# Kernel optimization log

Measured on AMD Instinct MI355X. Metric: run time of the kernel, lower is better.

The kernel has to match this reference:

```python
import jax, jax.numpy as jnp
import numpy as np

DIM = 128
N_GNN = 3
B, N1, N2 = 8, 128, 512
VDW_N = 6.0
DEV_VDW = 0.2
MAX_VDW, MIN_VDW = 0.0356, 0.0178
DM_MIN = 0.5


def setup_inputs() -> dict:
    key = jax.random.key(0)
    ks = jax.random.split(key, 24)
    f32 = jnp.float32
    h1 = jax.random.normal(ks[0], (B, N1, 54), f32)
    h2 = jax.random.normal(ks[1], (B, N2, 54), f32)
    a1 = (jax.random.uniform(ks[2], (B, N1, N1)) < 0.1).astype(f32)
    adj1 = jnp.clip(a1 + jnp.swapaxes(a1, 1, 2) + jnp.eye(N1, dtype=f32), 0.0, 1.0)
    a2 = (jax.random.uniform(ks[3], (B, N2, N2)) < 0.05).astype(f32)
    adj2 = jnp.clip(a2 + jnp.swapaxes(a2, 1, 2) + jnp.eye(N2, dtype=f32), 0.0, 1.0)
    A_int = (jax.random.uniform(ks[4], (B, 8, N1, N2)) < 0.05).astype(f32)
    pos1 = jax.random.uniform(ks[5], (B, N1, 3), f32) * 30.0
    pos2 = jax.random.uniform(ks[6], (B, N2, 3), f32) * 30.0
    rotor = jax.random.uniform(ks[7], (B,), f32) * 10.0
    vdw_radius1 = 1.0 + jax.random.uniform(ks[8], (B, N1), f32)
    vdw_radius2 = 1.0 + jax.random.uniform(ks[9], (B, N2), f32)
    delta_uff = jax.random.uniform(ks[10], (B,), f32)
    no_metal1 = jnp.ones((B, N1), f32)
    no_metal2 = jnp.ones((B, N2), f32)
    s = 0.1
    node_W = jax.random.normal(ks[11], (54, DIM), f32) * s
    gat_W = jax.random.normal(ks[12], (N_GNN, DIM, DIM), f32) * s
    gat_b = jnp.zeros((N_GNN, DIM), f32)
    gat_A = jax.random.normal(ks[13], (N_GNN, DIM, DIM), f32) * s
    gate_W = jax.random.normal(ks[14], (N_GNN, 2 * DIM), f32) * s
    gate_b = jnp.zeros((N_GNN,), f32)
    vdwA_W1 = jax.random.normal(ks[15], (2 * DIM, 128), f32) * s
    vdwA_b1 = jnp.zeros((128,), f32)
    vdwA_W2 = jax.random.normal(ks[16], (128,), f32) * s
    vdwA_b2 = jnp.zeros((1,), f32)
    vdwB_W1 = jax.random.normal(ks[17], (2 * DIM, 128), f32) * s
    vdwB_b1 = jnp.zeros((128,), f32)
    vdwB_W2 = jax.random.normal(ks[18], (128,), f32) * s
    vdwB_b2 = jnp.zeros((1,), f32)
    hbond_coeff = jnp.array([1.0], f32)
    hydrophobic_coeff = jnp.array([0.5], f32)
    vdw_coeff = jnp.array([1.0], f32)
    rotor_coeff = jnp.array([0.5], f32)
    return dict(h1=h1, adj1=adj1, h2=h2, adj2=adj2, A_int=A_int, pos1=pos1, pos2=pos2,
                rotor=rotor, vdw_radius1=vdw_radius1, vdw_radius2=vdw_radius2,
                delta_uff=delta_uff, no_metal1=no_metal1, no_metal2=no_metal2,
                node_W=node_W, gat_W=gat_W, gat_b=gat_b, gat_A=gat_A, gate_W=gate_W,
                gate_b=gate_b, vdwA_W1=vdwA_W1, vdwA_b1=vdwA_b1, vdwA_W2=vdwA_W2,
                vdwA_b2=vdwA_b2, vdwB_W1=vdwB_W1, vdwB_b1=vdwB_b1, vdwB_W2=vdwB_W2,
                vdwB_b2=vdwB_b2, hbond_coeff=hbond_coeff,
                hydrophobic_coeff=hydrophobic_coeff, vdw_coeff=vdw_coeff,
                rotor_coeff=rotor_coeff)


def _gat(x, adj, W, b, A, gW, gb):
    # PIGNet GAT_gate: attention softmax over axis=1, masked by adj, gated residual.
    h = x @ W + b                                   # [B,N,D]
    e = jnp.einsum('bil,bkl->bik', h @ A, h)        # [B,N,N]
    e = e + jnp.swapaxes(e, 1, 2)
    att = jnp.where(adj > 0, e, -9e15)
    att = jax.nn.softmax(att, axis=1) * adj
    h_prime = jax.nn.relu(jnp.einsum('bij,bjk->bik', att, h))
    coeff = jax.nn.sigmoid(jnp.concatenate([x, h_prime], -1) @ gW + gb)[..., None]
    return coeff * x + (1.0 - coeff) * h_prime


def _pair_mlp(g1, g2, W1, b1, w2, b2):
    # Equivalent to Linear(cat[h1_rep,h2_rep]) without materializing the 2D concat.
    z = (jnp.einsum('bik,kh->bih', g1, W1[:DIM])[:, :, None, :]
         + jnp.einsum('bjk,kh->bjh', g2, W1[DIM:])[:, None, :, :] + b1)  # [B,N1,N2,128]
    return jax.nn.relu(z) @ w2 + b2                 # [B,N1,N2]


def _forward(h1, adj1, h2, adj2, A_int, pos1, pos2, rotor, vdw_radius1, vdw_radius2,
             delta_uff, no_metal1, no_metal2, node_W, gat_W, gat_b, gat_A, gate_W,
             gate_b, vdwA_W1, vdwA_b1, vdwA_W2, vdwA_b2, vdwB_W1, vdwB_b1, vdwB_W2,
             vdwB_b2, hbond_coeff, hydrophobic_coeff, vdw_coeff, rotor_coeff):
    g1 = h1 @ node_W
    g2 = h2 @ node_W
    for i in range(N_GNN):
        g1 = _gat(g1, adj1, gat_W[i], gat_b[i], gat_A[i], gate_W[i], gate_b[i])
        g2 = _gat(g2, adj2, gat_W[i], gat_b[i], gat_A[i], gate_W[i], gate_b[i])
    diff = pos1[:, :, None, :] - pos2[:, None, :, :]
    dm = jnp.sqrt(jnp.sum(diff * diff, -1) + 1e-10)   # [B,N1,N2]
    dm = jnp.where(dm < DM_MIN, 1e10, dm)
    A_w = jax.nn.sigmoid(_pair_mlp(g1, g2, vdwA_W1, vdwA_b1, vdwA_W2, vdwA_b2))
    B_w = jnp.tanh(_pair_mlp(g1, g2, vdwB_W1, vdwB_b1, vdwB_W2, vdwB_b2)) * DEV_VDW
    dm0 = vdw_radius1[:, :, None] + vdw_radius2[:, None, :] + B_w
    # vdW 12-6 term
    dm0_safe = jnp.where(dm0 < 1e-4, 1.0, dm0)
    rN = (dm0_safe / dm) ** VDW_N
    evdw = jnp.minimum(rN * rN - 2.0 * rN, 100.0)
    mask12 = no_metal1[:, :, None] * no_metal2[:, None, :]
    Aamp = A_w * (MAX_VDW - MIN_VDW) + MIN_VDW
    E_vdw = jnp.sum(Aamp * evdw * mask12, axis=(1, 2))
    # hbond / hydrophobic terms use unfixed dm0
    dmd = dm - dm0
    hb = -(hbond_coeff * hbond_coeff)[0]
    hy = -(hydrophobic_coeff * hydrophobic_coeff)[0]
    E_hb1 = jnp.sum(jnp.clip(dmd * A_int[:, 1] / -0.7, 0.0, 1.0), axis=(1, 2)) * hb
    E_hb2 = jnp.sum(jnp.clip(dmd * A_int[:, -1] / -0.7, 0.0, 1.0), axis=(1, 2)) * hb
    E_hp = jnp.sum(jnp.clip((-dmd + 1.5) * A_int[:, -2], 0.0, 1.0), axis=(1, 2)) * hy
    E_t = delta_uff * (vdw_coeff * vdw_coeff)[0]
    ret = jnp.stack([E_vdw, E_hb1, E_hb2, E_hp, E_t], -1)   # [B,5]
    ret = ret / (1.0 + (rotor_coeff * rotor_coeff)[0] * rotor[:, None])
    return ret


def reference(h1, adj1, h2, adj2, A_int, pos1, pos2, rotor, vdw_radius1, vdw_radius2,
              delta_uff, no_metal1, no_metal2, node_W, gat_W, gat_b, gat_A, gate_W,
              gate_b, vdwA_W1, vdwA_b1, vdwA_W2, vdwA_b2, vdwB_W1, vdwB_b1, vdwB_W2,
              vdwB_b2, hbond_coeff, hydrophobic_coeff, vdw_coeff, rotor_coeff):
    return _forward(h1, adj1, h2, adj2, A_int, pos1, pos2, rotor, vdw_radius1,
                    vdw_radius2, delta_uff, no_metal1, no_metal2, node_W, gat_W,
                    gat_b, gat_A, gate_W, gate_b, vdwA_W1, vdwA_b1, vdwA_W2,
                    vdwA_b2, vdwB_W1, vdwB_b1, vdwB_W2, vdwB_b2, hbond_coeff,
                    hydrophobic_coeff, vdw_coeff, rotor_coeff)
```

## Files before the change

kernel.cpp:

```cpp
#include <hip/hip_runtime.h>
#include <math.h>

#define D 128
#define NB 8
#define NN1 128
#define NN2 512
#define ROWS1 (NB * NN1)
#define ROWS2 (NB * NN2)
#define ROWS (ROWS1 + ROWS2)
#define CAP1 96
#define CAP2 160
#define CSR_ELEMS ((size_t)ROWS1 * CAP1 + (size_t)ROWS2 * CAP2)

__device__ __forceinline__ void resolve_row(int row, int& base_row, size_t& cbase,
                                            int& N) {
    if (row < ROWS1) {
        base_row = row & ~127;
        cbase = (size_t)row * CAP1;
        N = NN1;
    } else {
        int r = row - ROWS1;
        base_row = ROWS1 + (r & ~511);
        cbase = (size_t)ROWS1 * CAP1 + (size_t)r * CAP2;
        N = NN2;
    }
}

__global__ __launch_bounds__(128) void k_csrembed(
    const float* __restrict__ h1, const float* __restrict__ h2,
    const float* __restrict__ adj1, const float* __restrict__ adj2,
    const float* __restrict__ W, float* __restrict__ g,
    unsigned short* __restrict__ csr, int* __restrict__ nnz) {
    int row = blockIdx.x;
    int t = threadIdx.x;
    const float* src = (row < ROWS1) ? h1 + (size_t)row * 54
                                     : h2 + (size_t)(row - ROWS1) * 54;
    __shared__ float xr[56];
    if (t < 54) xr[t] = src[t];
    __syncthreads();
    float a0 = 0.f, a1 = 0.f;
#pragma unroll
    for (int k = 0; k < 54; k += 2) {
        a0 += xr[k] * W[k * D + t];
        if (k + 1 < 54) a1 += xr[k + 1] * W[(k + 1) * D + t];
    }
    g[(size_t)row * D + t] = a0 + a1;

    if (t < 64) {
        int base_row, N;
        size_t cbase;
        resolve_row(row, base_row, cbase, N);
        int cap = (row < ROWS1) ? CAP1 : CAP2;
        const float* arow = (row < ROWS1)
                                ? adj1 + (size_t)row * NN1
                                : adj2 + (size_t)(row - ROWS1) * NN2;
        int cnt = 0;
        for (int c0 = 0; c0 < N; c0 += 64) {
            float v = arow[c0 + t];
            unsigned long long m = __ballot(v > 0.f);
            int rank = __popcll(m & ((1ull << t) - 1ull));
            if (v > 0.f && cnt + rank < cap)
                csr[cbase + cnt + rank] = (unsigned short)(c0 + t);
            cnt += __popcll(m);
        }
        if (t == 0) nnz[row] = cnt < cap ? cnt : cap;
    }
}

__global__ __launch_bounds__(256) void k_h(const float* __restrict__ g,
                                           const float* __restrict__ W,
                                           const float* __restrict__ bias,
                                           const float* __restrict__ A,
                                           float* __restrict__ h, float* __restrict__ hA) {
    int row0 = blockIdx.x * 16;
    int t = threadIdx.x;
    int d = t & 127, rh = t >> 7;
    __shared__ float xs[16][D];
    __shared__ float hs[16][D];
    {
        int r = t >> 4, c = (t & 15) * 8;
        *(float4*)&xs[r][c] = *(const float4*)&g[((size_t)row0 + r) * D + c];
        *(float4*)&xs[r][c + 4] = *(const float4*)&g[((size_t)row0 + r) * D + c + 4];
    }
    __syncthreads();
    float bv = bias[d];
    float acc[8];
#pragma unroll
    for (int u = 0; u < 8; ++u) acc[u] = bv;
    for (int k0 = 0; k0 < D; k0 += 4) {
        float w0 = W[(k0 + 0) * D + d];
        float w1 = W[(k0 + 1) * D + d];
        float w2 = W[(k0 + 2) * D + d];
        float w3 = W[(k0 + 3) * D + d];
#pragma unroll
        for (int u = 0; u < 8; ++u) {
            float4 xv = *(const float4*)&xs[rh * 8 + u][k0];
            acc[u] += xv.x * w0 + xv.y * w1 + xv.z * w2 + xv.w * w3;
        }
    }
#pragma unroll
    for (int u = 0; u < 8; ++u) {
        int r = rh * 8 + u;
        h[((size_t)row0 + r) * D + d] = acc[u];
        hs[r][d] = acc[u];
    }
    __syncthreads();
    float acc2[8];
#pragma unroll
    for (int u = 0; u < 8; ++u) acc2[u] = 0.f;
    for (int k0 = 0; k0 < D; k0 += 4) {
        float w0 = A[(k0 + 0) * D + d];
        float w1 = A[(k0 + 1) * D + d];
        float w2 = A[(k0 + 2) * D + d];
        float w3 = A[(k0 + 3) * D + d];
#pragma unroll
        for (int u = 0; u < 8; ++u) {
            float4 xv = *(const float4*)&hs[rh * 8 + u][k0];
            acc2[u] += xv.x * w0 + xv.y * w1 + xv.z * w2 + xv.w * w3;
        }
    }
#pragma unroll
    for (int u = 0; u < 8; ++u)
        hA[((size_t)row0 + rh * 8 + u) * D + d] = acc2[u];
}

__global__ __launch_bounds__(128) void k_Ssp(const float* __restrict__ h,
                                             const float* __restrict__ hA,
                                             const unsigned short* __restrict__ csr,
                                             const int* __restrict__ nnz,
                                             float* __restrict__ svals,
                                             float2* __restrict__ rowstat) {
    int row = blockIdx.x;
    int t = threadIdx.x;
    int base_row, N;
    size_t cbase;
    resolve_row(row, base_row, cbase, N);
    int n = nnz[row];
    int grp = t >> 4, u = t & 15;
    const float* hrow = h + (size_t)row * D + u * 8;
    const float* hArow = hA + (size_t)row * D + u * 8;
    float4 hi0 = *(const float4*)&hrow[0], hi1 = *(const float4*)&hrow[4];
    float4 ai0 = *(const float4*)&hArow[0], ai1 = *(const float4*)&hArow[4];
    __shared__ float sv[CAP2];
    for (int s0 = 0; s0 < n; s0 += 8) {
        int s = s0 + grp;
        float p = 0.f;
        if (s < n) {
            int jrow = base_row + csr[cbase + s];
            const float* hj = h + (size_t)jrow * D + u * 8;
            const float* aj = hA + (size_t)jrow * D + u * 8;
            float4 hj0 = *(const float4*)&hj[0], hj1 = *(const float4*)&hj[4];
            float4 aj0 = *(const float4*)&aj[0], aj1 = *(const float4*)&aj[4];
            p = hi0.x * aj0.x + hi0.y * aj0.y + hi0.z * aj0.z + hi0.w * aj0.w +
                hi1.x * aj1.x + hi1.y * aj1.y + hi1.z * aj1.z + hi1.w * aj1.w +
                ai0.x * hj0.x + ai0.y * hj0.y + ai0.z * hj0.z + ai0.w * hj0.w +
                ai1.x * hj1.x + ai1.y * hj1.y + ai1.z * hj1.z + ai1.w * hj1.w;
        }
#pragma unroll
        for (int o = 8; o > 0; o >>= 1) p += __shfl_xor(p, o);
        if (s < n && u == 0) sv[s] = p;
    }
    __syncthreads();
    if (t < 64) {
        float m = -3.4e38f;
        for (int s = t; s < n; s += 64) m = fmaxf(m, sv[s]);
#pragma unroll
        for (int o = 32; o > 0; o >>= 1) m = fmaxf(m, __shfl_xor(m, o));
        float sum = 0.f;
        for (int s = t; s < n; s += 64) sum += expf(sv[s] - m);
#pragma unroll
        for (int o = 32; o > 0; o >>= 1) sum += __shfl_xor(sum, o);
        if (t == 0) rowstat[row] = make_float2(m, 1.f / sum);
    }
    for (int s = t; s < n; s += 128) svals[cbase + s] = sv[s];
}

__global__ __launch_bounds__(128) void k_hpgate(const float* __restrict__ hbuf,
                                                float* __restrict__ g,
                                                const float* __restrict__ svals,
                                                const float2* __restrict__ rowstat,
                                                const unsigned short* __restrict__ csr,
                                                const int* __restrict__ nnz,
                                                const float* __restrict__ gW,
                                                const float* __restrict__ gb) {
    int row = blockIdx.x;
    int d = threadIdx.x;
    int base_row, N;
    size_t cbase;
    resolve_row(row, base_row, cbase, N);
    int n = nnz[row];
    __shared__ float avals[CAP2];
    __shared__ int aidx[CAP2];
    __shared__ float red[128];
    for (int s = d; s < n; s += 128) {
        int jrow = base_row + csr[cbase + s];
        float2 st = rowstat[jrow];
        avals[s] = expf(svals[cbase + s] - st.x) * st.y;
        aidx[s] = jrow;
    }
    __syncthreads();
    float a0 = 0.f, a1 = 0.f, a2 = 0.f, a3 = 0.f;
    int s = 0;
    for (; s + 4 <= n; s += 4) {
        a0 += avals[s + 0] * hbuf[(size_t)aidx[s + 0] * D + d];
        a1 += avals[s + 1] * hbuf[(size_t)aidx[s + 1] * D + d];
        a2 += avals[s + 2] * hbuf[(size_t)aidx[s + 2] * D + d];
        a3 += avals[s + 3] * hbuf[(size_t)aidx[s + 3] * D + d];
    }
    for (; s < n; ++s) a0 += avals[s] * hbuf[(size_t)aidx[s] * D + d];
    float hv = fmaxf(a0 + a1 + a2 + a3, 0.f);
    float xv = g[(size_t)row * D + d];
    red[d] = xv * gW[d] + hv * gW[D + d];
    __syncthreads();
    for (int o = 64; o > 0; o >>= 1) {
        if (d < o) red[d] += red[d + o];
        __syncthreads();
    }
    float c = 1.f / (1.f + expf(-(red[0] + gb[0])));
    g[(size_t)row * D + d] = c * xv + (1.f - c) * hv;
}

__global__ __launch_bounds__(256) void k_pairpre(const float* __restrict__ g,
                                                 const float* __restrict__ WA,
                                                 const float* __restrict__ WB,
                                                 const float* __restrict__ bA,
                                                 const float* __restrict__ bB,
                                                 float* __restrict__ aA,
                                                 float* __restrict__ aB) {
    int row0 = blockIdx.x * 16;
    int t = threadIdx.x;
    int d = t & 127, rh = t >> 7;
    int g2 = (row0 >= ROWS1);
    const float* WAp = g2 ? WA + D * D : WA;
    const float* WBp = g2 ? WB + D * D : WB;
    __shared__ float xs[16][D];
    {
        int r = t >> 4, c = (t & 15) * 8;
        *(float4*)&xs[r][c] = *(const float4*)&g[((size_t)row0 + r) * D + c];
        *(float4*)&xs[r][c + 4] = *(const float4*)&g[((size_t)row0 + r) * D + c + 4];
    }
    __syncthreads();
    float bvA = g2 ? 0.f : bA[d];
    float bvB = g2 ? 0.f : bB[d];
    float accA[8], accB[8];
#pragma unroll
    for (int u = 0; u < 8; ++u) { accA[u] = bvA; accB[u] = bvB; }
    for (int k0 = 0; k0 < D; k0 += 4) {
        float wa0 = WAp[(k0 + 0) * D + d], wa1 = WAp[(k0 + 1) * D + d];
        float wa2 = WAp[(k0 + 2) * D + d], wa3 = WAp[(k0 + 3) * D + d];
        float wb0 = WBp[(k0 + 0) * D + d], wb1 = WBp[(k0 + 1) * D + d];
        float wb2 = WBp[(k0 + 2) * D + d], wb3 = WBp[(k0 + 3) * D + d];
#pragma unroll
        for (int u = 0; u < 8; ++u) {
            float4 xv = *(const float4*)&xs[rh * 8 + u][k0];
            accA[u] += xv.x * wa0 + xv.y * wa1 + xv.z * wa2 + xv.w * wa3;
            accB[u] += xv.x * wb0 + xv.y * wb1 + xv.z * wb2 + xv.w * wb3;
        }
    }
#pragma unroll
    for (int u = 0; u < 8; ++u) {
        int r = rh * 8 + u;
        aA[((size_t)row0 + r) * D + d] = accA[u];
        aB[((size_t)row0 + r) * D + d] = accB[u];
    }
}

__global__ __launch_bounds__(256) void k_pairz(
    const float* __restrict__ aA, const float* __restrict__ aB,
    const float* __restrict__ w2A, const float* __restrict__ w2B,
    const float* __restrict__ b2A, const float* __restrict__ b2B,
    const float* __restrict__ pos1, const float* __restrict__ pos2,
    const float* __restrict__ vr1, const float* __restrict__ vr2,
    const float* __restrict__ nm1, const float* __restrict__ nm2,
    const float* __restrict__ A_int, float* __restrict__ partials) {
    int b = blockIdx.y;
    int itile = blockIdx.x >> 4, jtile = blockIdx.x & 15;
    int i0 = itile * 32, j0 = jtile * 32;
    int t = threadIdx.x;
    int tx = t & 15, ty = t >> 4;
    __shared__ float A1a[32][20], A1b[32][20], A2a[32][20], A2b[32][20];
    __shared__ float w2As[128], w2Bs[128];
    __shared__ float zAs[32][33], zBs[32][33];
    if (t < 128) { w2As[t] = w2A[t]; w2Bs[t] = w2B[t]; }
    float zA[2][2] = {{0.f, 0.f}, {0.f, 0.f}};
    float zB[2][2] = {{0.f, 0.f}, {0.f, 0.f}};
    int half = t >> 7, idx = t & 127;
    int sr = idx >> 2, sc = (idx & 3) * 4;
    size_t grow = half ? (size_t)(ROWS1 + b * NN2 + j0 + sr)
                       : (size_t)(b * NN1 + i0 + sr);
    for (int hc = 0; hc < D; hc += 16) {
        __syncthreads();
        float4 va = *(const float4*)&aA[grow * D + hc + sc];
        float4 vb = *(const float4*)&aB[grow * D + hc + sc];
        if (half) { *(float4*)&A2a[sr][sc] = va; *(float4*)&A2b[sr][sc] = vb; }
        else      { *(float4*)&A1a[sr][sc] = va; *(float4*)&A1b[sr][sc] = vb; }
        __syncthreads();
#pragma unroll
        for (int hh = 0; hh < 16; hh += 4) {
            float4 wA = *(const float4*)&w2As[hc + hh];
            float4 wB = *(const float4*)&w2Bs[hc + hh];
            float4 xA0 = *(const float4*)&A1a[ty][hh];
            float4 xA1 = *(const float4*)&A1a[ty + 16][hh];
            float4 xB0 = *(const float4*)&A1b[ty][hh];
            float4 xB1 = *(const float4*)&A1b[ty + 16][hh];
            float4 yA0 = *(const float4*)&A2a[tx][hh];
            float4 yA1 = *(const float4*)&A2a[tx + 16][hh];
            float4 yB0 = *(const float4*)&A2b[tx][hh];
            float4 yB1 = *(const float4*)&A2b[tx + 16][hh];
#define RD4(xx, yy, ww) (fmaxf(xx.x + yy.x, 0.f) * ww.x + fmaxf(xx.y + yy.y, 0.f) * ww.y + \
                         fmaxf(xx.z + yy.z, 0.f) * ww.z + fmaxf(xx.w + yy.w, 0.f) * ww.w)
            zA[0][0] += RD4(xA0, yA0, wA); zA[0][1] += RD4(xA0, yA1, wA);
            zA[1][0] += RD4(xA1, yA0, wA); zA[1][1] += RD4(xA1, yA1, wA);
            zB[0][0] += RD4(xB0, yB0, wB); zB[0][1] += RD4(xB0, yB1, wB);
            zB[1][0] += RD4(xB1, yB0, wB); zB[1][1] += RD4(xB1, yB1, wB);
#undef RD4
        }
    }
#pragma unroll
    for (int u = 0; u < 2; ++u)
#pragma unroll
        for (int v = 0; v < 2; ++v) {
            zAs[ty + 16 * u][tx + 16 * v] = zA[u][v];
            zBs[ty + 16 * u][tx + 16 * v] = zB[u][v];
        }
    __syncthreads();
    int j2 = t & 31, ig = t >> 5;
    int jg = j0 + j2;
    size_t j_off = (size_t)b * NN2 + jg;
    float p2x = pos2[j_off * 3 + 0], p2y = pos2[j_off * 3 + 1], p2z = pos2[j_off * 3 + 2];
    float r2 = vr2[j_off], m2 = nm2[j_off];
    float zb2A = b2A[0], zb2B = b2B[0];
    float eV[4], e1[4], e2[4], eH[4];
#pragma unroll
    for (int ii = 0; ii < 4; ++ii) {
        int il = ig * 4 + ii;
        int iglob = i0 + il;
        size_t i_off = (size_t)b * NN1 + iglob;
        float zAv = zAs[il][j2] + zb2A;
        float zBv = zBs[il][j2] + zb2B;
        float dx = pos1[i_off * 3 + 0] - p2x;
        float dy = pos1[i_off * 3 + 1] - p2y;
        float dz = pos1[i_off * 3 + 2] - p2z;
        float dm = sqrtf(dx * dx + dy * dy + dz * dz + 1e-10f);
        if (dm < 0.5f) dm = 1e10f;
        float A_w = 1.f / (1.f + expf(-zAv));
        float B_w = tanhf(zBv) * 0.2f;
        float dm0 = vr1[i_off] + r2 + B_w;
        float dm0s = (dm0 < 1e-4f) ? 1.f : dm0;
        float rr = dm0s / dm;
        float rr2 = rr * rr;
        float rN = rr2 * rr2 * rr2;
        float evdw = fminf(rN * rN - 2.f * rN, 100.f);
        float mask = nm1[i_off] * m2;
        float Aamp = A_w * (0.0356f - 0.0178f) + 0.0178f;
        eV[ii] = Aamp * evdw * mask;
        float dmd = dm - dm0;
        size_t abase = (((size_t)b * 8) * NN1 + iglob) * NN2 + jg;
        float Ai1 = A_int[abase + (size_t)1 * NN1 * NN2];
        float Ai6 = A_int[abase + (size_t)6 * NN1 * NN2];
        float Ai7 = A_int[abase + (size_t)7 * NN1 * NN2];
        e1[ii] = fminf(fmaxf(dmd * Ai1 * (-1.f / 0.7f), 0.f), 1.f);
        e2[ii] = fminf(fmaxf(dmd * Ai7 * (-1.f / 0.7f), 0.f), 1.f);
        eH[ii] = fminf(fmaxf((1.5f - dmd) * Ai6, 0.f), 1.f);
    }
#pragma unroll
    for (int o = 16; o > 0; o >>= 1) {
#pragma unroll
        for (int ii = 0; ii < 4; ++ii) {
            eV[ii] += __shfl_xor(eV[ii], o);
            e1[ii] += __shfl_xor(e1[ii], o);
            e2[ii] += __shfl_xor(e2[ii], o);
            eH[ii] += __shfl_xor(eH[ii], o);
        }
    }
    if (j2 == 0) {
#pragma unroll
        for (int ii = 0; ii < 4; ++ii) {
            int iglob = i0 + ig * 4 + ii;
            float* pp = partials + (((size_t)b * NN1 + iglob) * 16 + jtile) * 4;
            pp[0] = eV[ii]; pp[1] = e1[ii]; pp[2] = e2[ii]; pp[3] = eH[ii];
        }
    }
}

__global__ void k_final(const float* __restrict__ partials, const float* __restrict__ rotor,
                        const float* __restrict__ duff, const float* __restrict__ hbond,
                        const float* __restrict__ hydro, const float* __restrict__ vdwc,
                        const float* __restrict__ rotc, float* __restrict__ out) {
    int b = blockIdx.x;
    int t = threadIdx.x;
    __shared__ float r[4][128];
    float v0 = 0.f, v1 = 0.f, v2 = 0.f, v3 = 0.f;
    const float* p = partials + ((size_t)b * NN1 + t) * 16 * 4;
#pragma unroll
    for (int jt = 0; jt < 16; ++jt) {
        v0 += p[jt * 4 + 0]; v1 += p[jt * 4 + 1];
        v2 += p[jt * 4 + 2]; v3 += p[jt * 4 + 3];
    }
    r[0][t] = v0; r[1][t] = v1; r[2][t] = v2; r[3][t] = v3;
    __syncthreads();
    for (int s = 64; s > 0; s >>= 1) {
        if (t < s) {
            r[0][t] += r[0][t + s];
            r[1][t] += r[1][t + s];
            r[2][t] += r[2][t + s];
            r[3][t] += r[3][t + s];
        }
        __syncthreads();
    }
    if (t == 0) {
        float hb = -hbond[0] * hbond[0];
        float hy = -hydro[0] * hydro[0];
        float Et = duff[b] * vdwc[0] * vdwc[0];
        float sc = 1.f / (1.f + rotc[0] * rotc[0] * rotor[b]);
        out[b * 5 + 0] = r[0][0] * sc;
        out[b * 5 + 1] = r[1][0] * hb * sc;
        out[b * 5 + 2] = r[2][0] * hb * sc;
        out[b * 5 + 3] = r[3][0] * hy * sc;
        out[b * 5 + 4] = Et * sc;
    }
}

extern "C" void kernel_launch(void* const* d_in, const int* in_sizes, int n_in,
                              void* d_out, int out_size, void* d_ws, size_t ws_size,
                              hipStream_t stream) {
    const float* h1    = (const float*)d_in[0];
    const float* adj1  = (const float*)d_in[1];
    const float* h2    = (const float*)d_in[2];
    const float* adj2  = (const float*)d_in[3];
    const float* A_int = (const float*)d_in[4];
    const float* pos1  = (const float*)d_in[5];
    const float* pos2  = (const float*)d_in[6];
    const float* rotor = (const float*)d_in[7];
    const float* vr1   = (const float*)d_in[8];
    const float* vr2   = (const float*)d_in[9];
    const float* duff  = (const float*)d_in[10];
    const float* nm1   = (const float*)d_in[11];
    const float* nm2   = (const float*)d_in[12];
    const float* nodeW = (const float*)d_in[13];
    const float* gatW  = (const float*)d_in[14];
    const float* gatb  = (const float*)d_in[15];
    const float* gatA  = (const float*)d_in[16];
    const float* gateW = (const float*)d_in[17];
    const float* gateb = (const float*)d_in[18];
    const float* vA_W1 = (const float*)d_in[19];
    const float* vA_b1 = (const float*)d_in[20];
    const float* vA_W2 = (const float*)d_in[21];
    const float* vA_b2 = (const float*)d_in[22];
    const float* vB_W1 = (const float*)d_in[23];
    const float* vB_b1 = (const float*)d_in[24];
    const float* vB_W2 = (const float*)d_in[25];
    const float* vB_b2 = (const float*)d_in[26];
    const float* hbond = (const float*)d_in[27];
    const float* hydro = (const float*)d_in[28];
    const float* vdwc  = (const float*)d_in[29];
    const float* rotc  = (const float*)d_in[30];

    float* p = (float*)d_ws;
    float* g     = p; p += (size_t)ROWS * D;
    float* hbuf  = p; p += (size_t)ROWS * D;
    float* hAbuf = p; p += (size_t)ROWS * D;
    float* svals = p; p += CSR_ELEMS;
    float2* rowstat = (float2*)p; p += 2 * (size_t)ROWS;
    float* partials = p; p += (size_t)NB * NN1 * 16 * 4;
    unsigned short* csr = (unsigned short*)p;
    int* nnz = (int*)(csr + CSR_ELEMS);
    float* aA = hbuf;
    float* aB = hAbuf;

    k_csrembed<<<ROWS, 128, 0, stream>>>(h1, h2, adj1, adj2, nodeW, g, csr, nnz);

    for (int l = 0; l < 3; ++l) {
        const float* W  = gatW  + (size_t)l * D * D;
        const float* bb = gatb  + (size_t)l * D;
        const float* A  = gatA  + (size_t)l * D * D;
        const float* gW = gateW + (size_t)l * 2 * D;
        const float* gb = gateb + l;
        k_h<<<ROWS / 16, 256, 0, stream>>>(g, W, bb, A, hbuf, hAbuf);
        k_Ssp<<<ROWS, 128, 0, stream>>>(hbuf, hAbuf, csr, nnz, svals, rowstat);
        k_hpgate<<<ROWS, 128, 0, stream>>>(hbuf, g, svals, rowstat, csr, nnz, gW, gb);
    }

    k_pairpre<<<ROWS / 16, 256, 0, stream>>>(g, vA_W1, vB_W1, vA_b1, vB_b1, aA, aB);
    k_pairz<<<dim3(64, NB), 256, 0, stream>>>(aA, aB, vA_W2, vB_W2, vA_b2, vB_b2,
                                              pos1, pos2, vr1, vr2, nm1, nm2, A_int,
                                              partials);
    k_final<<<NB, 128, 0, stream>>>(partials, rotor, duff, hbond, hydro, vdwc, rotc,
                                    (float*)d_out);
}
```

Before: 312.6 us.

## Fuse all stages into one persistent cooperative kernel with grid syncs

Replaces the sequence of about a dozen kernel launches (CSR build, three GAT layers of three kernels each, pair precompute, pair energy, final reduction) with a single cooperative persistent kernel. Each phase loops over work items with a grid-stride loop and phases are separated by grid.sync(). This removes per-launch overhead and inter-kernel gaps, but pays for roughly a dozen grid-wide barriers. It also processes two rows per 256-thread block and caps the grid at the occupancy limit, up to 1024 blocks, which may lower the parallelism available in some phases.

```diff
diff --git a/kernel.cpp b/kernel.cpp
--- a/kernel.cpp
+++ b/kernel.cpp
@@ -1,5 +1,8 @@
 #include <hip/hip_runtime.h>
+#include <hip/hip_cooperative_groups.h>
 #include <math.h>
+
+namespace cg = cooperative_groups;
 
 #define D 128
 #define NB 8
@@ -11,6 +14,17 @@
 #define CAP1 96
 #define CAP2 160
 #define CSR_ELEMS ((size_t)ROWS1 * CAP1 + (size_t)ROWS2 * CAP2)
+
+struct KParams {
+    const float *h1, *adj1, *h2, *adj2, *A_int, *pos1, *pos2, *rotor, *vr1, *vr2,
+                *duff, *nm1, *nm2, *nodeW, *gatW, *gatb, *gatA, *gateW, *gateb,
+                *vA_W1, *vA_b1, *vA_W2, *vA_b2, *vB_W1, *vB_b1, *vB_W2, *vB_b2,
+                *hbond, *hydro, *vdwc, *rotc;
+    float *g, *hbuf, *hAbuf, *svals, *partials, *out;
+    float2 *rowstat;
+    unsigned short *csr;
+    int *nnz;
+};
 
 __device__ __forceinline__ void resolve_row(int row, int& base_row, size_t& cbase,
                                             int& N) {
@@ -26,465 +40,451 @@
     }
 }
 
-__global__ __launch_bounds__(128) void k_csrembed(
-    const float* __restrict__ h1, const float* __restrict__ h2,
-    const float* __restrict__ adj1, const float* __restrict__ adj2,
-    const float* __restrict__ W, float* __restrict__ g,
-    unsigned short* __restrict__ csr, int* __restrict__ nnz) {
-    int row = blockIdx.x;
-    int t = threadIdx.x;
-    const float* src = (row < ROWS1) ? h1 + (size_t)row * 54
-                                     : h2 + (size_t)(row - ROWS1) * 54;
-    __shared__ float xr[56];
-    if (t < 54) xr[t] = src[t];
-    __syncthreads();
-    float a0 = 0.f, a1 = 0.f;
-#pragma unroll
-    for (int k = 0; k < 54; k += 2) {
-        a0 += xr[k] * W[k * D + t];
-        if (k + 1 < 54) a1 += xr[k + 1] * W[(k + 1) * D + t];
-    }
-    g[(size_t)row * D + t] = a0 + a1;
-
-    if (t < 64) {
-        int base_row, N;
-        size_t cbase;
-        resolve_row(row, base_row, cbase, N);
-        int cap = (row < ROWS1) ? CAP1 : CAP2;
-        const float* arow = (row < ROWS1)
-                                ? adj1 + (size_t)row * NN1
-                                : adj2 + (size_t)(row - ROWS1) * NN2;
-        int cnt = 0;
-        for (int c0 = 0; c0 < N; c0 += 64) {
-            float v = arow[c0 + t];
-            unsigned long long m = __ballot(v > 0.f);
-            int rank = __popcll(m & ((1ull << t) - 1ull));
-            if (v > 0.f && cnt + rank < cap)
-                csr[cbase + cnt + rank] = (unsigned short)(c0 + t);
-            cnt += __popcll(m);
-        }
-        if (t == 0) nnz[row] = cnt < cap ? cnt : cap;
-    }
-}
-
-__global__ __launch_bounds__(256) void k_h(const float* __restrict__ g,
-                                           const float* __restrict__ W,
-                                           const float* __restrict__ bias,
-                                           const float* __restrict__ A,
-                                           float* __restrict__ h, float* __restrict__ hA) {
-    int row0 = blockIdx.x * 16;
-    int t = threadIdx.x;
-    int d = t & 127, rh = t >> 7;
-    __shared__ float xs[16][D];
-    __shared__ float hs[16][D];
-    {
-        int r = t >> 4, c = (t & 15) * 8;
-        *(float4*)&xs[r][c] = *(const float4*)&g[((size_t)row0 + r) * D + c];
-        *(float4*)&xs[r][c + 4] = *(const float4*)&g[((size_t)row0 + r) * D + c + 4];
-    }
-    __syncthreads();
-    float bv = bias[d];
-    float acc[8];
-#pragma unroll
-    for (int u = 0; u < 8; ++u) acc[u] = bv;
-    for (int k0 = 0; k0 < D; k0 += 4) {
-        float w0 = W[(k0 + 0) * D + d];
-        float w1 = W[(k0 + 1) * D + d];
-        float w2 = W[(k0 + 2) * D + d];
-        float w3 = W[(k0 + 3) * D + d];
+__global__ __launch_bounds__(256, 4) void k_mega(KParams pp) {
+    cg::grid_group grid = cg::this_grid();
+    const int t = threadIdx.x;
+    const int bid = blockIdx.x;
+    const int G = gridDim.x;
+
+    __shared__ union SMem {
+        struct { float xr[2][56]; } p0;
+        struct { float xs[16][D]; float hs[16][D]; } ph;
+        struct { float sv[2][CAP2]; } pb;
+        struct { float avals[2][CAP2]; int aidx[2][CAP2]; float red[256]; } pc;
+        struct { float A1a[32][20], A1b[32][20], A2a[32][20], A2b[32][20];
+                 float w2As[D], w2Bs[D], zAs[32][33], zBs[32][33]; } pe;
+        struct { float r[4][128]; } pf;
+    } sm;
+
+    for (int r0 = bid * 2; r0 < ROWS; r0 += 2 * G) {
+        __syncthreads();
+        int half = t >> 7, t2 = t & 127;
+        int row = r0 + half;
+        const float* src = (row < ROWS1) ? pp.h1 + (size_t)row * 54
+                                         : pp.h2 + (size_t)(row - ROWS1) * 54;
+        if (t2 < 54) sm.p0.xr[half][t2] = src[t2];
+        __syncthreads();
+        float a0 = 0.f, a1 = 0.f;
+#pragma unroll
+        for (int k = 0; k < 54; k += 2) {
+            a0 += sm.p0.xr[half][k] * pp.nodeW[k * D + t2];
+            if (k + 1 < 54) a1 += sm.p0.xr[half][k + 1] * pp.nodeW[(k + 1) * D + t2];
+        }
+        pp.g[(size_t)row * D + t2] = a0 + a1;
+        if (t2 < 64) {
+            int base_row, N; size_t cbase;
+            resolve_row(row, base_row, cbase, N);
+            int cap = (row < ROWS1) ? CAP1 : CAP2;
+            const float* arow = (row < ROWS1)
+                                    ? pp.adj1 + (size_t)row * NN1
+                                    : pp.adj2 + (size_t)(row - ROWS1) * NN2;
+            int cnt = 0;
+            for (int c0 = 0; c0 < N; c0 += 64) {
+                float v = arow[c0 + t2];
+                unsigned long long m = __ballot(v > 0.f);
+                int rank = __popcll(m & ((1ull << t2) - 1ull));
+                if (v > 0.f && cnt + rank < cap)
+                    pp.csr[cbase + cnt + rank] = (unsigned short)(c0 + t2);
+                cnt += __popcll(m);
+            }
+            if (t2 == 0) pp.nnz[row] = cnt < cap ? cnt : cap;
+        }
+    }
+    grid.sync();
+
+    for (int l = 0; l < 3; ++l) {
+        const float* W  = pp.gatW  + (size_t)l * D * D;
+        const float* bb = pp.gatb  + (size_t)l * D;
+        const float* A  = pp.gatA  + (size_t)l * D * D;
+        const float* gW = pp.gateW + (size_t)l * 2 * D;
+        const float  gb0 = pp.gateb[l];
+
+        for (int grp = bid; grp < ROWS / 16; grp += G) {
+            __syncthreads();
+            int row0 = grp * 16;
+            int d = t & 127, rh = t >> 7;
+            {
+                int r = t >> 4, c = (t & 15) * 8;
+                *(float4*)&sm.ph.xs[r][c] = *(const float4*)&pp.g[((size_t)row0 + r) * D + c];
+                *(float4*)&sm.ph.xs[r][c + 4] = *(const float4*)&pp.g[((size_t)row0 + r) * D + c + 4];
+            }
+            __syncthreads();
+            float bv = bb[d];
+            float acc[8];
+#pragma unroll
+            for (int u = 0; u < 8; ++u) acc[u] = bv;
+            for (int k0 = 0; k0 < D; k0 += 4) {
+                float w0 = W[(k0 + 0) * D + d];
+                float w1 = W[(k0 + 1) * D + d];
+                float w2 = W[(k0 + 2) * D + d];
+                float w3 = W[(k0 + 3) * D + d];
+#pragma unroll
+                for (int u = 0; u < 8; ++u) {
+                    float4 xv = *(const float4*)&sm.ph.xs[rh * 8 + u][k0];
+                    acc[u] += xv.x * w0 + xv.y * w1 + xv.z * w2 + xv.w * w3;
+                }
+            }
+#pragma unroll
+            for (int u = 0; u < 8; ++u) {
+                int r = rh * 8 + u;
+                pp.hbuf[((size_t)row0 + r) * D + d] = acc[u];
+                sm.ph.hs[r][d] = acc[u];
+            }
+            __syncthreads();
+            float acc2[8];
+#pragma unroll
+            for (int u = 0; u < 8; ++u) acc2[u] = 0.f;
+            for (int k0 = 0; k0 < D; k0 += 4) {
+                float w0 = A[(k0 + 0) * D + d];
+                float w1 = A[(k0 + 1) * D + d];
+                float w2 = A[(k0 + 2) * D + d];
+                float w3 = A[(k0 + 3) * D + d];
+#pragma unroll
+                for (int u = 0; u < 8; ++u) {
+                    float4 xv = *(const float4*)&sm.ph.hs[rh * 8 + u][k0];
+                    acc2[u] += xv.x * w0 + xv.y * w1 + xv.z * w2 + xv.w * w3;
+                }
+            }
+#pragma unroll
+            for (int u = 0; u < 8; ++u)
+                pp.hAbuf[((size_t)row0 + rh * 8 + u) * D + d] = acc2[u];
+        }
+        grid.sync();
+
+        for (int r0 = bid * 2; r0 < ROWS; r0 += 2 * G) {
+            __syncthreads();
+            int half = t >> 7, t2 = t & 127;
+            int row = r0 + half;
+            int base_row, N; size_t cbase;
+            resolve_row(row, base_row, cbase, N);
+            int n = pp.nnz[row];
+            int grp8 = t2 >> 4, u = t2 & 15;
+            const float* hrow = pp.hbuf + (size_t)row * D + u * 8;
+            const float* hArow = pp.hAbuf + (size_t)row * D + u * 8;
+            float4 hi0 = *(const float4*)&hrow[0], hi1 = *(const float4*)&hrow[4];
+            float4 ai0 = *(const float4*)&hArow[0], ai1 = *(const float4*)&hArow[4];
+            float* sv = sm.pb.sv[half];
+            for (int s0 = 0; s0 < n; s0 += 8) {
+                int s = s0 + grp8;
+                float pv = 0.f;
+                if (s < n) {
+                    int jrow = base_row + pp.csr[cbase + s];
+                    const float* hj = pp.hbuf + (size_t)jrow * D + u * 8;
+                    const float* aj = pp.hAbuf + (size_t)jrow * D + u * 8;
+                    float4 hj0 = *(const float4*)&hj[0], hj1 = *(const float4*)&hj[4];
+                    float4 aj0 = *(const float4*)&aj[0], aj1 = *(const float4*)&aj[4];
+                    pv = hi0.x * aj0.x + hi0.y * aj0.y + hi0.z * aj0.z + hi0.w * aj0.w +
+                         hi1.x * aj1.x + hi1.y * aj1.y + hi1.z * aj1.z + hi1.w * aj1.w +
+                         ai0.x * hj0.x + ai0.y * hj0.y + ai0.z * hj0.z + ai0.w * hj0.w +
+                         ai1.x * hj1.x + ai1.y * hj1.y + ai1.z * hj1.z + ai1.w * hj1.w;
+                }
+                pv += __shfl_xor(pv, 8);
+                pv += __shfl_xor(pv, 4);
+                pv += __shfl_xor(pv, 2);
+                pv += __shfl_xor(pv, 1);
+                if (s < n && u == 0) sv[s] = pv;
+            }
+            __syncthreads();
+            if (t2 < 64) {
+                float m = -3.4e38f;
+                for (int s = t2; s < n; s += 64) m = fmaxf(m, sv[s]);
+#pragma unroll
+                for (int o = 32; o > 0; o >>= 1) m = fmaxf(m, __shfl_xor(m, o));
+                float sum = 0.f;
+                for (int s = t2; s < n; s += 64) sum += expf(sv[s] - m);
+#pragma unroll
+                for (int o = 32; o > 0; o >>= 1) sum += __shfl_xor(sum, o);
+                if (t2 == 0) pp.rowstat[row] = make_float2(m, 1.f / sum);
+            }
+            for (int s = t2; s < n; s += 128) pp.svals[cbase + s] = sv[s];
+        }
+        grid.sync();
+
+        for (int r0 = bid * 2; r0 < ROWS; r0 += 2 * G) {
+            __syncthreads();
+            int half = t >> 7, d = t & 127;
+            int row = r0 + half;
+            int base_row, N; size_t cbase;
+            resolve_row(row, base_row, cbase, N);
+            int n = pp.nnz[row];
+            float* avals = sm.pc.avals[half];
+            int* aidx = sm.pc.aidx[half];
+            for (int s = d; s < n; s += 128) {
+                int jrow = base_row + pp.csr[cbase + s];
+                float2 st = pp.rowstat[jrow];
+                avals[s] = expf(pp.svals[cbase + s] - st.x) * st.y;
+                aidx[s] = jrow;
+            }
+            __syncthreads();
+            float a0 = 0.f, a1 = 0.f, a2 = 0.f, a3 = 0.f;
+            int s = 0;
+            for (; s + 4 <= n; s += 4) {
+                a0 += avals[s + 0] * pp.hbuf[(size_t)aidx[s + 0] * D + d];
+                a1 += avals[s + 1] * pp.hbuf[(size_t)aidx[s + 1] * D + d];
+                a2 += avals[s + 2] * pp.hbuf[(size_t)aidx[s + 2] * D + d];
+                a3 += avals[s + 3] * pp.hbuf[(size_t)aidx[s + 3] * D + d];
+            }
+            for (; s < n; ++s) a0 += avals[s] * pp.hbuf[(size_t)aidx[s] * D + d];
+            float hv = fmaxf(a0 + a1 + a2 + a3, 0.f);
+            float xv = pp.g[(size_t)row * D + d];
+            sm.pc.red[t] = xv * gW[d] + hv * gW[D + d];
+            __syncthreads();
+            for (int o = 64; o > 0; o >>= 1) {
+                if ((t & 127) < o) sm.pc.red[t] += sm.pc.red[t + o];
+                __syncthreads();
+            }
+            float c = 1.f / (1.f + expf(-(sm.pc.red[half * 128] + gb0)));
+            pp.g[(size_t)row * D + d] = c * xv + (1.f - c) * hv;
+        }
+        grid.sync();
+    }
+
+    for (int grp = bid; grp < ROWS / 16; grp += G) {
+        __syncthreads();
+        int row0 = grp * 16;
+        int d = t & 127, rh = t >> 7;
+        int g2 = (row0 >= ROWS1);
+        const float* WAp = g2 ? pp.vA_W1 + D * D : pp.vA_W1;
+        const float* WBp = g2 ? pp.vB_W1 + D * D : pp.vB_W1;
+        {
+            int r = t >> 4, c = (t & 15) * 8;
+            *(float4*)&sm.ph.xs[r][c] = *(const float4*)&pp.g[((size_t)row0 + r) * D + c];
+            *(float4*)&sm.ph.xs[r][c + 4] = *(const float4*)&pp.g[((size_t)row0 + r) * D + c + 4];
+        }
+        __syncthreads();
+        float bvA = g2 ? 0.f : pp.vA_b1[d];
+        float bvB = g2 ? 0.f : pp.vB_b1[d];
+        float accA[8], accB[8];
+#pragma unroll
+        for (int u = 0; u < 8; ++u) { accA[u] = bvA; accB[u] = bvB; }
+        for (int k0 = 0; k0 < D; k0 += 4) {
+            float wa0 = WAp[(k0 + 0) * D + d], wa1 = WAp[(k0 + 1) * D + d];
+            float wa2 = WAp[(k0 + 2) * D + d], wa3 = WAp[(k0 + 3) * D + d];
+            float wb0 = WBp[(k0 + 0) * D + d], wb1 = WBp[(k0 + 1) * D + d];
+            float wb2 = WBp[(k0 + 2) * D + d], wb3 = WBp[(k0 + 3) * D + d];
+#pragma unroll
+            for (int u = 0; u < 8; ++u) {
+                float4 xv = *(const float4*)&sm.ph.xs[rh * 8 + u][k0];
+                accA[u] += xv.x * wa0 + xv.y * wa1 + xv.z * wa2 + xv.w * wa3;
+                accB[u] += xv.x * wb0 + xv.y * wb1 + xv.z * wb2 + xv.w * wb3;
+            }
+        }
 #pragma unroll
         for (int u = 0; u < 8; ++u) {
-            float4 xv = *(const float4*)&xs[rh * 8 + u][k0];
-            acc[u] += xv.x * w0 + xv.y * w1 + xv.z * w2 + xv.w * w3;
-        }
-    }
-#pragma unroll
-    for (int u = 0; u < 8; ++u) {
-        int r = rh * 8 + u;
-        h[((size_t)row0 + r) * D + d] = acc[u];
-        hs[r][d] = acc[u];
-    }
-    __syncthreads();
-    float acc2[8];
-#pragma unroll
-    for (int u = 0; u < 8; ++u) acc2[u] = 0.f;
-    for (int k0 = 0; k0 < D; k0 += 4) {
-        float w0 = A[(k0 + 0) * D + d];
-        float w1 = A[(k0 + 1) * D + d];
-        float w2 = A[(k0 + 2) * D + d];
-        float w3 = A[(k0 + 3) * D + d];
-#pragma unroll
-        for (int u = 0; u < 8; ++u) {
-            float4 xv = *(const float4*)&hs[rh * 8 + u][k0];
-            acc2[u] += xv.x * w0 + xv.y * w1 + xv.z * w2 + xv.w * w3;
-        }
-    }
-#pragma unroll
-    for (int u = 0; u < 8; ++u)
-        hA[((size_t)row0 + rh * 8 + u) * D + d] = acc2[u];
-}
-
-__global__ __launch_bounds__(128) void k_Ssp(const float* __restrict__ h,
-                                             const float* __restrict__ hA,
-                                             const unsigned short* __restrict__ csr,
-                                             const int* __restrict__ nnz,
-                                             float* __restrict__ svals,
-                                             float2* __restrict__ rowstat) {
-    int row = blockIdx.x;
-    int t = threadIdx.x;
-    int base_row, N;
-    size_t cbase;
-    resolve_row(row, base_row, cbase, N);
-    int n = nnz[row];
-    int grp = t >> 4, u = t & 15;
-    const float* hrow = h + (size_t)row * D + u * 8;
-    const float* hArow = hA + (size_t)row * D + u * 8;
-    float4 hi0 = *(const float4*)&hrow[0], hi1 = *(const float4*)&hrow[4];
-    float4 ai0 = *(const float4*)&hArow[0], ai1 = *(const float4*)&hArow[4];
-    __shared__ float sv[CAP2];
-    for (int s0 = 0; s0 < n; s0 += 8) {
-        int s = s0 + grp;
-        float p = 0.f;
-        if (s < n) {
-            int jrow = base_row + csr[cbase + s];
-            const float* hj = h + (size_t)jrow * D + u * 8;
-            const float* aj = hA + (size_t)jrow * D + u * 8;
-            float4 hj0 = *(const float4*)&hj[0], hj1 = *(const float4*)&hj[4];
-            float4 aj0 = *(const float4*)&aj[0], aj1 = *(const float4*)&aj[4];
-            p = hi0.x * aj0.x + hi0.y * aj0.y + hi0.z * aj0.z + hi0.w * aj0.w +
-                hi1.x * aj1.x + hi1.y * aj1.y + hi1.z * aj1.z + hi1.w * aj1.w +
-                ai0.x * hj0.x + ai0.y * hj0.y + ai0.z * hj0.z + ai0.w * hj0.w +
-                ai1.x * hj1.x + ai1.y * hj1.y + ai1.z * hj1.z + ai1.w * hj1.w;
-        }
-#pragma unroll
-        for (int o = 8; o > 0; o >>= 1) p += __shfl_xor(p, o);
-        if (s < n && u == 0) sv[s] = p;
-    }
-    __syncthreads();
-    if (t < 64) {
-        float m = -3.4e38f;
-        for (int s = t; s < n; s += 64) m = fmaxf(m, sv[s]);
-#pragma unroll
-        for (int o = 32; o > 0; o >>= 1) m = fmaxf(m, __shfl_xor(m, o));
-        float sum = 0.f;
-        for (int s = t; s < n; s += 64) sum += expf(sv[s] - m);
-#pragma unroll
-        for (int o = 32; o > 0; o >>= 1) sum += __shfl_xor(sum, o);
-        if (t == 0) rowstat[row] = make_float2(m, 1.f / sum);
-    }
-    for (int s = t; s < n; s += 128) svals[cbase + s] = sv[s];
-}
-
-__global__ __launch_bounds__(128) void k_hpgate(const float* __restrict__ hbuf,
-                                                float* __restrict__ g,
-                                                const float* __restrict__ svals,
-                                                const float2* __restrict__ rowstat,
-                                                const unsigned short* __restrict__ csr,
-                                                const int* __restrict__ nnz,
-                                                const float* __restrict__ gW,
-                                                const float* __restrict__ gb) {
-    int row = blockIdx.x;
-    int d = threadIdx.x;
-    int base_row, N;
-    size_t cbase;
-    resolve_row(row, base_row, cbase, N);
-    int n = nnz[row];
-    __shared__ float avals[CAP2];
-    __shared__ int aidx[CAP2];
-    __shared__ float red[128];
-    for (int s = d; s < n; s += 128) {
-        int jrow = base_row + csr[cbase + s];
-        float2 st = rowstat[jrow];
-        avals[s] = expf(svals[cbase + s] - st.x) * st.y;
-        aidx[s] = jrow;
-    }
-    __syncthreads();
-    float a0 = 0.f, a1 = 0.f, a2 = 0.f, a3 = 0.f;
-    int s = 0;
-    for (; s + 4 <= n; s += 4) {
-        a0 += avals[s + 0] * hbuf[(size_t)aidx[s + 0] * D + d];
-        a1 += avals[s + 1] * hbuf[(size_t)aidx[s + 1] * D + d];
-        a2 += avals[s + 2] * hbuf[(size_t)aidx[s + 2] * D + d];
-        a3 += avals[s + 3] * hbuf[(size_t)aidx[s + 3] * D + d];
-    }
-    for (; s < n; ++s) a0 += avals[s] * hbuf[(size_t)aidx[s] * D + d];
-    float hv = fmaxf(a0 + a1 + a2 + a3, 0.f);
-    float xv = g[(size_t)row * D + d];
-    red[d] = xv * gW[d] + hv * gW[D + d];
-    __syncthreads();
-    for (int o = 64; o > 0; o >>= 1) {
-        if (d < o) red[d] += red[d + o];
-        __syncthreads();
-    }
-    float c = 1.f / (1.f + expf(-(red[0] + gb[0])));
-    g[(size_t)row * D + d] = c * xv + (1.f - c) * hv;
-}
-
-__global__ __launch_bounds__(256) void k_pairpre(const float* __restrict__ g,
-                                                 const float* __restrict__ WA,
-                                                 const float* __restrict__ WB,
-                                                 const float* __restrict__ bA,
-                                                 const float* __restrict__ bB,
-                                                 float* __restrict__ aA,
-                                                 float* __restrict__ aB) {
-    int row0 = blockIdx.x * 16;
-    int t = threadIdx.x;
-    int d = t & 127, rh = t >> 7;
-    int g2 = (row0 >= ROWS1);
-    const float* WAp = g2 ? WA + D * D : WA;
-    const float* WBp = g2 ? WB + D * D : WB;
-    __shared__ float xs[16][D];
-    {
-        int r = t >> 4, c = (t & 15) * 8;
-        *(float4*)&xs[r][c] = *(const float4*)&g[((size_t)row0 + r) * D + c];
-        *(float4*)&xs[r][c + 4] = *(const float4*)&g[((size_t)row0 + r) * D + c + 4];
-    }
-    __syncthreads();
-    float bvA = g2 ? 0.f : bA[d];
-    float bvB = g2 ? 0.f : bB[d];
-    float accA[8], accB[8];
-#pragma unroll
-    for (int u = 0; u < 8; ++u) { accA[u] = bvA; accB[u] = bvB; }
-    for (int k0 = 0; k0 < D; k0 += 4) {
-        float wa0 = WAp[(k0 + 0) * D + d], wa1 = WAp[(k0 + 1) * D + d];
-        float wa2 = WAp[(k0 + 2) * D + d], wa3 = WAp[(k0 + 3) * D + d];
-        float wb0 = WBp[(k0 + 0) * D + d], wb1 = WBp[(k0 + 1) * D + d];
-        float wb2 = WBp[(k0 + 2) * D + d], wb3 = WBp[(k0 + 3) * D + d];
-#pragma unroll
-        for (int u = 0; u < 8; ++u) {
-            float4 xv = *(const float4*)&xs[rh * 8 + u][k0];
-            accA[u] += xv.x * wa0 + xv.y * wa1 + xv.z * wa2 + xv.w * wa3;
-            accB[u] += xv.x * wb0 + xv.y * wb1 + xv.z * wb2 + xv.w * wb3;
-        }
-    }
-#pragma unroll
-    for (int u = 0; u < 8; ++u) {
-        int r = rh * 8 + u;
-        aA[((size_t)row0 + r) * D + d] = accA[u];
-        aB[((size_t)row0 + r) * D + d] = accB[u];
-    }
-}
-
-__global__ __launch_bounds__(256) void k_pairz(
-    const float* __restrict__ aA, const float* __restrict__ aB,
-    const float* __restrict__ w2A, const float* __restrict__ w2B,
-    const float* __restrict__ b2A, const float* __restrict__ b2B,
-    const float* __restrict__ pos1, const float* __restrict__ pos2,
-    const float* __restrict__ vr1, const float* __restrict__ vr2,
-    const float* __restrict__ nm1, const float* __restrict__ nm2,
-    const float* __restrict__ A_int, float* __restrict__ partials) {
-    int b = blockIdx.y;
-    int itile = blockIdx.x >> 4, jtile = blockIdx.x & 15;
-    int i0 = itile * 32, j0 = jtile * 32;
-    int t = threadIdx.x;
-    int tx = t & 15, ty = t >> 4;
-    __shared__ float A1a[32][20], A1b[32][20], A2a[32][20], A2b[32][20];
-    __shared__ float w2As[128], w2Bs[128];
-    __shared__ float zAs[32][33], zBs[32][33];
-    if (t < 128) { w2As[t] = w2A[t]; w2Bs[t] = w2B[t]; }
-    float zA[2][2] = {{0.f, 0.f}, {0.f, 0.f}};
-    float zB[2][2] = {{0.f, 0.f}, {0.f, 0.f}};
-    int half = t >> 7, idx = t & 127;
-    int sr = idx >> 2, sc = (idx & 3) * 4;
-    size_t grow = half ? (size_t)(ROWS1 + b * NN2 + j0 + sr)
-                       : (size_t)(b * NN1 + i0 + sr);
-    for (int hc = 0; hc < D; hc += 16) {
-        __syncthreads();
-        float4 va = *(const float4*)&aA[grow * D + hc + sc];
-        float4 vb = *(const float4*)&aB[grow * D + hc + sc];
-        if (half) { *(float4*)&A2a[sr][sc] = va; *(float4*)&A2b[sr][sc] = vb; }
-        else      { *(float4*)&A1a[sr][sc] = va; *(float4*)&A1b[sr][sc] = vb; }
-        __syncthreads();
-#pragma unroll
-        for (int hh = 0; hh < 16; hh += 4) {
-            float4 wA = *(const float4*)&w2As[hc + hh];
-            float4 wB = *(const float4*)&w2Bs[hc + hh];
-            float4 xA0 = *(const float4*)&A1a[ty][hh];
-            float4 xA1 = *(const float4*)&A1a[ty + 16][hh];
-            float4 xB0 = *(const float4*)&A1b[ty][hh];
-            float4 xB1 = *(const float4*)&A1b[ty + 16][hh];
-            float4 yA0 = *(const float4*)&A2a[tx][hh];
-            float4 yA1 = *(const float4*)&A2a[tx + 16][hh];
-            float4 yB0 = *(const float4*)&A2b[tx][hh];
-            float4 yB1 = *(const float4*)&A2b[tx + 16][hh];
+            int r = rh * 8 + u;
+            pp.hbuf[((size_t)row0 + r) * D + d] = accA[u];
+            pp.hAbuf[((size_t)row0 + r) * D + d] = accB[u];
+        }
+    }
+    grid.sync();
+
+    for (int tile = bid; tile < 512; tile += G) {
+        int b = tile >> 6;
+        int itile = (tile >> 4) & 3, jtile = tile & 15;
+        int i0 = itile * 32, j0 = jtile * 32;
+        int tx = t & 15, ty = t >> 4;
+        if (t < 128) { sm.pe.w2As[t] = pp.vA_W2[t]; sm.pe.w2Bs[t] = pp.vB_W2[t]; }
+        float zA[2][2] = {{0.f, 0.f}, {0.f, 0.f}};
+        float zB[2][2] = {{0.f, 0.f}, {0.f, 0.f}};
+        int half = t >> 7, idx = t & 127;
+        int sr = idx >> 2, sc = (idx & 3) * 4;
+        size_t grow = half ? (size_t)(ROWS1 + b * NN2 + j0 + sr)
+                           : (size_t)(b * NN1 + i0 + sr);
+        for (int hc = 0; hc < D; hc += 16) {
+            __syncthreads();
+            float4 va = *(const float4*)&pp.hbuf[grow * D + hc + sc];
+            float4 vb = *(const float4*)&pp.hAbuf[grow * D + hc + sc];
+            if (half) { *(float4*)&sm.pe.A2a[sr][sc] = va; *(float4*)&sm.pe.A2b[sr][sc] = vb; }
+            else      { *(float4*)&sm.pe.A1a[sr][sc] = va; *(float4*)&sm.pe.A1b[sr][sc] = vb; }
+            __syncthreads();
+#pragma unroll
+            for (int hh = 0; hh < 16; hh += 4) {
+                float4 wA = *(const float4*)&sm.pe.w2As[hc + hh];
+                float4 wB = *(const float4*)&sm.pe.w2Bs[hc + hh];
+                float4 xA0 = *(const float4*)&sm.pe.A1a[ty][hh];
+                float4 xA1 = *(const float4*)&sm.pe.A1a[ty + 16][hh];
+                float4 xB0 = *(const float4*)&sm.pe.A1b[ty][hh];
+                float4 xB1 = *(const float4*)&sm.pe.A1b[ty + 16][hh];
+                float4 yA0 = *(const float4*)&sm.pe.A2a[tx][hh];
+                float4 yA1 = *(const float4*)&sm.pe.A2a[tx + 16][hh];
+                float4 yB0 = *(const float4*)&sm.pe.A2b[tx][hh];
+                float4 yB1 = *(const float4*)&sm.pe.A2b[tx + 16][hh];
 #define RD4(xx, yy, ww) (fmaxf(xx.x + yy.x, 0.f) * ww.x + fmaxf(xx.y + yy.y, 0.f) * ww.y + \
                          fmaxf(xx.z + yy.z, 0.f) * ww.z + fmaxf(xx.w + yy.w, 0.f) * ww.w)
-            zA[0][0] += RD4(xA0, yA0, wA); zA[0][1] += RD4(xA0, yA1, wA);
-            zA[1][0] += RD4(xA1, yA0, wA); zA[1][1] += RD4(xA1, yA1, wA);
-            zB[0][0] += RD4(xB0, yB0, wB); zB[0][1] += RD4(xB0, yB1, wB);
-            zB[1][0] += RD4(xB1, yB0, wB); zB[1][1] += RD4(xB1, yB1, wB);
+                zA[0][0] += RD4(xA0, yA0, wA); zA[0][1] += RD4(xA0, yA1, wA);
+                zA[1][0] += RD4(xA1, yA0, wA); zA[1][1] += RD4(xA1, yA1, wA);
+                zB[0][0] += RD4(xB0, yB0, wB); zB[0][1] += RD4(xB0, yB1, wB);
+                zB[1][0] += RD4(xB1, yB0, wB); zB[1][1] += RD4(xB1, yB1, wB);
 #undef RD4
-        }
-    }
-#pragma unroll
-    for (int u = 0; u < 2; ++u)
-#pragma unroll
-        for (int v = 0; v < 2; ++v) {
-            zAs[ty + 16 * u][tx + 16 * v] = zA[u][v];
-            zBs[ty + 16 * u][tx + 16 * v] = zB[u][v];
-        }
-    __syncthreads();
-    int j2 = t & 31, ig = t >> 5;
-    int jg = j0 + j2;
-    size_t j_off = (size_t)b * NN2 + jg;
-    float p2x = pos2[j_off * 3 + 0], p2y = pos2[j_off * 3 + 1], p2z = pos2[j_off * 3 + 2];
-    float r2 = vr2[j_off], m2 = nm2[j_off];
-    float zb2A = b2A[0], zb2B = b2B[0];
-    float eV[4], e1[4], e2[4], eH[4];
-#pragma unroll
-    for (int ii = 0; ii < 4; ++ii) {
-        int il = ig * 4 + ii;
-        int iglob = i0 + il;
-        size_t i_off = (size_t)b * NN1 + iglob;
-        float zAv = zAs[il][j2] + zb2A;
-        float zBv = zBs[il][j2] + zb2B;
-        float dx = pos1[i_off * 3 + 0] - p2x;
-        float dy = pos1[i_off * 3 + 1] - p2y;
-        float dz = pos1[i_off * 3 + 2] - p2z;
-        float dm = sqrtf(dx * dx + dy * dy + dz * dz + 1e-10f);
-        if (dm < 0.5f) dm = 1e10f;
-        float A_w = 1.f / (1.f + expf(-zAv));
-        float B_w = tanhf(zBv) * 0.2f;
-        float dm0 = vr1[i_off] + r2 + B_w;
-        float dm0s = (dm0 < 1e-4f) ? 1.f : dm0;
-        float rr = dm0s / dm;
-        float rr2 = rr * rr;
-        float rN = rr2 * rr2 * rr2;
-        float evdw = fminf(rN * rN - 2.f * rN, 100.f);
-        float mask = nm1[i_off] * m2;
-        float Aamp = A_w * (0.0356f - 0.0178f) + 0.0178f;
-        eV[ii] = Aamp * evdw * mask;
-        float dmd = dm - dm0;
-        size_t abase = (((size_t)b * 8) * NN1 + iglob) * NN2 + jg;
-        float Ai1 = A_int[abase + (size_t)1 * NN1 * NN2];
-        float Ai6 = A_int[abase + (size_t)6 * NN1 * NN2];
-        float Ai7 = A_int[abase + (size_t)7 * NN1 * NN2];
-        e1[ii] = fminf(fmaxf(dmd * Ai1 * (-1.f / 0.7f), 0.f), 1.f);
-        e2[ii] = fminf(fmaxf(dmd * Ai7 * (-1.f / 0.7f), 0.f), 1.f);
-        eH[ii] = fminf(fmaxf((1.5f - dmd) * Ai6, 0.f), 1.f);
-    }
-#pragma unroll
-    for (int o = 16; o > 0; o >>= 1) {
+            }
+        }
+#pragma unroll
+        for (int u = 0; u < 2; ++u)
+#pragma unroll
+            for (int v = 0; v < 2; ++v) {
+                sm.pe.zAs[ty + 16 * u][tx + 16 * v] = zA[u][v];
+                sm.pe.zBs[ty + 16 * u][tx + 16 * v] = zB[u][v];
+            }
+        __syncthreads();
+        int j2 = t & 31, ig = t >> 5;
+        int jg = j0 + j2;
+        size_t j_off = (size_t)b * NN2 + jg;
+        float p2x = pp.pos2[j_off * 3 + 0], p2y = pp.pos2[j_off * 3 + 1],
+              p2z = pp.pos2[j_off * 3 + 2];
+        float r2 = pp.vr2[j_off], m2 = pp.nm2[j_off];
+        float zb2A = pp.vA_b2[0], zb2B = pp.vB_b2[0];
+        float eV[4], e1[4], e2[4], eH[4];
 #pragma unroll
         for (int ii = 0; ii < 4; ++ii) {
-            eV[ii] += __shfl_xor(eV[ii], o);
-            e1[ii] += __shfl_xor(e1[ii], o);
-            e2[ii] += __shfl_xor(e2[ii], o);
-            eH[ii] += __shfl_xor(eH[ii], o);
-        }
-    }
-    if (j2 == 0) {
-#pragma unroll
-        for (int ii = 0; ii < 4; ++ii) {
-            int iglob = i0 + ig * 4 + ii;
-            float* pp = partials + (((size_t)b * NN1 + iglob) * 16 + jtile) * 4;
-            pp[0] = eV[ii]; pp[1] = e1[ii]; pp[2] = e2[ii]; pp[3] = eH[ii];
-        }
-    }
-}
-
-__global__ void k_final(const float* __restrict__ partials, const float* __restrict__ rotor,
-                        const float* __restrict__ duff, const float* __restrict__ hbond,
-                        const float* __restrict__ hydro, const float* __restrict__ vdwc,
-                        const float* __restrict__ rotc, float* __restrict__ out) {
-    int b = blockIdx.x;
-    int t = threadIdx.x;
-    __shared__ float r[4][128];
-    float v0 = 0.f, v1 = 0.f, v2 = 0.f, v3 = 0.f;
-    const float* p = partials + ((size_t)b * NN1 + t) * 16 * 4;
-#pragma unroll
-    for (int jt = 0; jt < 16; ++jt) {
-        v0 += p[jt * 4 + 0]; v1 += p[jt * 4 + 1];
-        v2 += p[jt * 4 + 2]; v3 += p[jt * 4 + 3];
-    }
-    r[0][t] = v0; r[1][t] = v1; r[2][t] = v2; r[3][t] = v3;
-    __syncthreads();
-    for (int s = 64; s > 0; s >>= 1) {
-        if (t < s) {
-            r[0][t] += r[0][t + s];
-            r[1][t] += r[1][t + s];
-            r[2][t] += r[2][t + s];
-            r[3][t] += r[3][t + s];
-        }
-        __syncthreads();
-    }
-    if (t == 0) {
-        float hb = -hbond[0] * hbond[0];
-        float hy = -hydro[0] * hydro[0];
-        float Et = duff[b] * vdwc[0] * vdwc[0];
-        float sc = 1.f / (1.f + rotc[0] * rotc[0] * rotor[b]);
-        out[b * 5 + 0] = r[0][0] * sc;
-        out[b * 5 + 1] = r[1][0] * hb * sc;
-        out[b * 5 + 2] = r[2][0] * hb * sc;
-        out[b * 5 + 3] = r[3][0] * hy * sc;
-        out[b * 5 + 4] = Et * sc;
+            int il = ig * 4 + ii;
+            int iglob = i0 + il;
+            size_t i_off = (size_t)b * NN1 + iglob;
+            float zAv = sm.pe.zAs[il][j2] + zb2A;
+            float zBv = sm.pe.zBs[il][j2] + zb2B;
+            float dx = pp.pos1[i_off * 3 + 0] - p2x;
+            float dy = pp.pos1[i_off * 3 + 1] - p2y;
+            float dz = pp.pos1[i_off * 3 + 2] - p2z;
+            float dm = sqrtf(dx * dx + dy * dy + dz * dz + 1e-10f);
+            if (dm < 0.5f) dm = 1e10f;
+            float A_w = 1.f / (1.f + expf(-zAv));
+            float B_w = tanhf(zBv) * 0.2f;
+            float dm0 = pp.vr1[i_off] + r2 + B_w;
+            float dm0s = (dm0 < 1e-4f) ? 1.f : dm0;
+            float rr = dm0s / dm;
+            float rr2 = rr * rr;
+            float rN = rr2 * rr2 * rr2;
+            float evdw = fminf(rN * rN - 2.f * rN, 100.f);
+            float mask = pp.nm1[i_off] * m2;
+            float Aamp = A_w * (0.0356f - 0.0178f) + 0.0178f;
+            eV[ii] = Aamp * evdw * mask;
+            float dmd = dm - dm0;
+            size_t abase = (((size_t)b * 8) * NN1 + iglob) * NN2 + jg;
+            float Ai1 = pp.A_int[abase + (size_t)1 * NN1 * NN2];
+            float Ai6 = pp.A_int[abase + (size_t)6 * NN1 * NN2];
+            float Ai7 = pp.A_int[abase + (size_t)7 * NN1 * NN2];
+            e1[ii] = fminf(fmaxf(dmd * Ai1 * (-1.f / 0.7f), 0.f), 1.f);
+            e2[ii] = fminf(fmaxf(dmd * Ai7 * (-1.f / 0.7f), 0.f), 1.f);
+            eH[ii] = fminf(fmaxf((1.5f - dmd) * Ai6, 0.f), 1.f);
+        }
+#pragma unroll
+        for (int o = 16; o > 0; o >>= 1) {
+#pragma unroll
+            for (int ii = 0; ii < 4; ++ii) {
+                eV[ii] += __shfl_xor(eV[ii], o);
+                e1[ii] += __shfl_xor(e1[ii], o);
+                e2[ii] += __shfl_xor(e2[ii], o);
+                eH[ii] += __shfl_xor(eH[ii], o);
+            }
+        }
+        if (j2 == 0) {
+#pragma unroll
+            for (int ii = 0; ii < 4; ++ii) {
+                int iglob = i0 + ig * 4 + ii;
+                float* po = pp.partials + (((size_t)b * NN1 + iglob) * 16 + jtile) * 4;
+                po[0] = eV[ii]; po[1] = e1[ii]; po[2] = e2[ii]; po[3] = eH[ii];
+            }
+        }
+        __syncthreads();
+    }
+    grid.sync();
+
+    if (bid < NB) {
+        int b = bid;
+        if (t < 128) {
+            float v0 = 0.f, v1 = 0.f, v2 = 0.f, v3 = 0.f;
+            const float* pr = pp.partials + ((size_t)b * NN1 + t) * 16 * 4;
+#pragma unroll
+            for (int jt = 0; jt < 16; ++jt) {
+                v0 += pr[jt * 4 + 0]; v1 += pr[jt * 4 + 1];
+                v2 += pr[jt * 4 + 2]; v3 += pr[jt * 4 + 3];
+            }
+            sm.pf.r[0][t] = v0; sm.pf.r[1][t] = v1;
+            sm.pf.r[2][t] = v2; sm.pf.r[3][t] = v3;
+        }
+        __syncthreads();
+        for (int s = 64; s > 0; s >>= 1) {
+            if (t < s) {
+                sm.pf.r[0][t] += sm.pf.r[0][t + s];
+                sm.pf.r[1][t] += sm.pf.r[1][t + s];
+                sm.pf.r[2][t] += sm.pf.r[2][t + s];
+                sm.pf.r[3][t] += sm.pf.r[3][t + s];
+            }
+            __syncthreads();
+        }
+        if (t == 0) {
+            float hb = -pp.hbond[0] * pp.hbond[0];
+            float hy = -pp.hydro[0] * pp.hydro[0];
+            float Et = pp.duff[b] * pp.vdwc[0] * pp.vdwc[0];
+            float scl = 1.f / (1.f + pp.rotc[0] * pp.rotc[0] * pp.rotor[b]);
+            pp.out[b * 5 + 0] = sm.pf.r[0][0] * scl;
+            pp.out[b * 5 + 1] = sm.pf.r[1][0] * hb * scl;
+            pp.out[b * 5 + 2] = sm.pf.r[2][0] * hb * scl;
+            pp.out[b * 5 + 3] = sm.pf.r[3][0] * hy * scl;
+            pp.out[b * 5 + 4] = Et * scl;
+        }
     }
 }
 
 extern "C" void kernel_launch(void* const* d_in, const int* in_sizes, int n_in,
                               void* d_out, int out_size, void* d_ws, size_t ws_size,
                               hipStream_t stream) {
-    const float* h1    = (const float*)d_in[0];
-    const float* adj1  = (const float*)d_in[1];
-    const float* h2    = (const float*)d_in[2];
-    const float* adj2  = (const float*)d_in[3];
-    const float* A_int = (const float*)d_in[4];
-    const float* pos1  = (const float*)d_in[5];
-    const float* pos2  = (const float*)d_in[6];
-    const float* rotor = (const float*)d_in[7];
-    const float* vr1   = (const float*)d_in[8];
-    const float* vr2   = (const float*)d_in[9];
-    const float* duff  = (const float*)d_in[10];
-    const float* nm1   = (const float*)d_in[11];
-    const float* nm2   = (const float*)d_in[12];
-    const float* nodeW = (const float*)d_in[13];
-    const float* gatW  = (const float*)d_in[14];
-    const float* gatb  = (const float*)d_in[15];
-    const float* gatA  = (const float*)d_in[16];
-    const float* gateW = (const float*)d_in[17];
-    const float* gateb = (const float*)d_in[18];
-    const float* vA_W1 = (const float*)d_in[19];
-    const float* vA_b1 = (const float*)d_in[20];
-    const float* vA_W2 = (const float*)d_in[21];
-    const float* vA_b2 = (const float*)d_in[22];
-    const float* vB_W1 = (const float*)d_in[23];
-    const float* vB_b1 = (const float*)d_in[24];
-    const float* vB_W2 = (const float*)d_in[25];
-    const float* vB_b2 = (const float*)d_in[26];
-    const float* hbond = (const float*)d_in[27];
-    const float* hydro = (const float*)d_in[28];
-    const float* vdwc  = (const float*)d_in[29];
-    const float* rotc  = (const float*)d_in[30];
+    KParams prm;
+    prm.h1    = (const float*)d_in[0];
+    prm.adj1  = (const float*)d_in[1];
+    prm.h2    = (const float*)d_in[2];
+    prm.adj2  = (const float*)d_in[3];
+    prm.A_int = (const float*)d_in[4];
+    prm.pos1  = (const float*)d_in[5];
+    prm.pos2  = (const float*)d_in[6];
+    prm.rotor = (const float*)d_in[7];
+    prm.vr1   = (const float*)d_in[8];
+    prm.vr2   = (const float*)d_in[9];
+    prm.duff  = (const float*)d_in[10];
+    prm.nm1   = (const float*)d_in[11];
+    prm.nm2   = (const float*)d_in[12];
+    prm.nodeW = (const float*)d_in[13];
+    prm.gatW  = (const float*)d_in[14];
+    prm.gatb  = (const float*)d_in[15];
+    prm.gatA  = (const float*)d_in[16];
+    prm.gateW = (const float*)d_in[17];
+    prm.gateb = (const float*)d_in[18];
+    prm.vA_W1 = (const float*)d_in[19];
+    prm.vA_b1 = (const float*)d_in[20];
+    prm.vA_W2 = (const float*)d_in[21];
+    prm.vA_b2 = (const float*)d_in[22];
+    prm.vB_W1 = (const float*)d_in[23];
+    prm.vB_b1 = (const float*)d_in[24];
+    prm.vB_W2 = (const float*)d_in[25];
+    prm.vB_b2 = (const float*)d_in[26];
+    prm.hbond = (const float*)d_in[27];
+    prm.hydro = (const float*)d_in[28];
+    prm.vdwc  = (const float*)d_in[29];
+    prm.rotc  = (const float*)d_in[30];
 
     float* p = (float*)d_ws;
-    float* g     = p; p += (size_t)ROWS * D;
-    float* hbuf  = p; p += (size_t)ROWS * D;
-    float* hAbuf = p; p += (size_t)ROWS * D;
-    float* svals = p; p += CSR_ELEMS;
-    float2* rowstat = (float2*)p; p += 2 * (size_t)ROWS;
-    float* partials = p; p += (size_t)NB * NN1 * 16 * 4;
-    unsigned short* csr = (unsigned short*)p;
-    int* nnz = (int*)(csr + CSR_ELEMS);
-    float* aA = hbuf;
-    float* aB = hAbuf;
-
-    k_csrembed<<<ROWS, 128, 0, stream>>>(h1, h2, adj1, adj2, nodeW, g, csr, nnz);
-
-    for (int l = 0; l < 3; ++l) {
-        const float* W  = gatW  + (size_t)l * D * D;
-        const float* bb = gatb  + (size_t)l * D;
-        const float* A  = gatA  + (size_t)l * D * D;
-        const float* gW = gateW + (size_t)l * 2 * D;
-        const float* gb = gateb + l;
-        k_h<<<ROWS / 16, 256, 0, stream>>>(g, W, bb, A, hbuf, hAbuf);
-        k_Ssp<<<ROWS, 128, 0, stream>>>(hbuf, hAbuf, csr, nnz, svals, rowstat);
-        k_hpgate<<<ROWS, 128, 0, stream>>>(hbuf, g, svals, rowstat, csr, nnz, gW, gb);
-    }
-
-    k_pairpre<<<ROWS / 16, 256, 0, stream>>>(g, vA_W1, vB_W1, vA_b1, vB_b1, aA, aB);
-    k_pairz<<<dim3(64, NB), 256, 0, stream>>>(aA, aB, vA_W2, vB_W2, vA_b2, vB_b2,
-                                              pos1, pos2, vr1, vr2, nm1, nm2, A_int,
-                                              partials);
-    k_final<<<NB, 128, 0, stream>>>(partials, rotor, duff, hbond, hydro, vdwc, rotc,
-                                    (float*)d_out);
+    prm.g     = p; p += (size_t)ROWS * D;
+    prm.hbuf  = p; p += (size_t)ROWS * D;
+    prm.hAbuf = p; p += (size_t)ROWS * D;
+    prm.svals = p; p += CSR_ELEMS;
+    prm.rowstat = (float2*)p; p += 2 * (size_t)ROWS;
+    prm.partials = p; p += (size_t)NB * NN1 * 16 * 4;
+    prm.csr = (unsigned short*)p;
+    prm.nnz = (int*)(prm.csr + CSR_ELEMS);
+    prm.out = (float*)d_out;
+
+    int dev = 0;
+    hipGetDevice(&dev);
+    hipDeviceProp_t props;
+    hipGetDeviceProperties(&props, dev);
+    int maxB = 0;
+    hipOccupancyMaxActiveBlocksPerMultiprocessor(&maxB,
+        reinterpret_cast<const void*>(k_mega), 256, 0);
+    if (maxB < 1) maxB = 1;
+    long long Gl = (long long)maxB * props.multiProcessorCount;
+    int G = (Gl > 1024) ? 1024 : (int)Gl;
+    if (G < NB) G = NB;
+
+    void* args[] = {(void*)&prm};
+    hipLaunchCooperativeKernel(reinterpret_cast<const void*>(k_mega),
+                               dim3(G), dim3(256), args, 0u, stream);
 }
```

After: 1.235 ms. +294.9%, slower.
